# Kernel optimization log

Measured on AMD Instinct MI355X. Metric: run time of the kernel, lower is better.

Reference implementation:

```python
import jax, jax.numpy as jnp
import numpy as np

EPS = 1e-6  # VN-ReLU direction-norm epsilon
K_NN = 16


def vec_linear(x, W):
    # x: (B, Cin, 3, ...), W: (Cout, Cin) -> (B, Cout, 3, ...)
    return jnp.einsum('oi,bi...->bo...', W, x)


def vec_lna(x, W, U):
    # VecLinear + VN-LeakyReLU(negative_slope=0) acting on vector dim (axis 2)
    p = jnp.einsum('oi,bi...->bo...', W, x)   # feature map
    d = jnp.einsum('oi,bi...->bo...', U, x)   # direction map
    dot = jnp.sum(p * d, axis=2, keepdims=True)
    dsq = jnp.sum(d * d, axis=2, keepdims=True)
    return jnp.where(dot >= 0, p, p - (dot / (dsq + EPS)) * d)


def setup_inputs() -> dict:
    B, N = 2, 4096
    h, c, L = 128, 128, 4
    ks = jax.random.split(jax.random.key(0), 8)
    s = lambda k, shape, fan: (jax.random.normal(k, shape, jnp.float32) / np.sqrt(fan)).astype(jnp.float32)
    return {
        'x': jax.random.normal(ks[0], (B, 3, N), jnp.float32),
        'W_in': s(ks[1], (h, 3), 3),
        'U_in': s(ks[2], (h, 3), 3),
        'Wl': s(ks[3], (L, h, h), h),
        'Ul': s(ks[4], (L, h, h), h),
        'Wg': s(ks[5], (L, h, 2 * h), 2 * h),
        'Ug': s(ks[6], (L, h, 2 * h), 2 * h),
        'W_out': s(ks[7], (c, L * h), L * h),
    }


def reference(x, W_in, U_in, Wl, Ul, Wg, Ug, W_out):
    B, _, N = x.shape
    K = K_NN
    pts = jnp.transpose(x, (0, 2, 1))                      # (B, N, 3)
    # squared euclidean distance (same KNN ordering as torch.cdist p=2 + topk smallest)
    sq = jnp.sum(pts * pts, axis=-1)                       # (B, N)
    d2 = sq[:, :, None] + sq[:, None, :] - 2.0 * jnp.einsum('bnd,bmd->bnm', pts, pts)
    _, idx = jax.lax.top_k(-d2, K)                         # (B, N, K) nearest, sorted
    neighbors = jax.vmap(lambda p, i: p[i])(pts, idx)      # (B, N, K, 3) gather
    neighbors = jnp.transpose(neighbors, (0, 3, 1, 2))[:, None]  # (B, 1, 3, N, K)

    x4 = x[:, None]                                        # (B, 1, 3, N)
    x_pad = jnp.broadcast_to(x4[..., None], neighbors.shape)
    # F.normalize(x, dim=2) with eps=1e-12 clamp
    x_dir = x4 / jnp.maximum(jnp.linalg.norm(x4, axis=2, keepdims=True), 1e-12)
    cross = jnp.cross(jnp.broadcast_to(x_dir[..., None], neighbors.shape), neighbors, axis=2)
    y = jnp.concatenate([cross, neighbors - x_pad, x_pad], axis=1)  # (B, 3, 3, N, K)

    h_feat = vec_lna(y, W_in, U_in)                        # (B, h, 3, N, K)
    h_feat = jnp.mean(h_feat, axis=-1)                     # meanpool over K -> (B, h, 3, N)

    y = h_feat
    feats = []
    for i in range(Wl.shape[0]):
        y = vec_lna(y, Wl[i], Ul[i])                       # (B, h, 3, N)
        yg = jnp.mean(y, axis=-1, keepdims=True)
        y = jnp.concatenate([y, jnp.broadcast_to(yg, y.shape)], axis=1)  # (B, 2h, 3, N)
        y = vec_lna(y, Wg[i], Ug[i])                       # (B, h, 3, N)
        feats.append(y)

    out = vec_linear(jnp.concatenate(feats, axis=1), W_out)  # (B, c, 3, N)
    return (jnp.mean(out, axis=-1), out)
```

## Files before the change

### kernel.cpp

```cpp
#include <hip/hip_runtime.h>
#include <hip/hip_bf16.h>
#include <cfloat>


typedef __attribute__((ext_vector_type(8))) short short8;
typedef __attribute__((ext_vector_type(4))) float f32x4;

__device__ __forceinline__ unsigned short f2bf(float f) {
    union { float f; unsigned u; } v; v.f = f;
    unsigned r = v.u + 0x7fffu + ((v.u >> 16) & 1u);
    return (unsigned short)(r >> 16);
}
__device__ __forceinline__ float bf2f(unsigned short h) {
    union { unsigned u; float f; } v; v.u = ((unsigned)h) << 16;
    return v.f;
}

__global__ __launch_bounds__(256) void setup_kernel(const float* __restrict__ x,
                                                    float4* __restrict__ pts4,
                                                    const float* __restrict__ Wl,
                                                    const float* __restrict__ Ul,
                                                    const float* __restrict__ Wg,
                                                    const float* __restrict__ Ug,
                                                    const float* __restrict__ Wout,
                                                    unsigned short* __restrict__ Ah,
                                                    unsigned short* __restrict__ Al,
                                                    int N, int B) {
    int t = blockIdx.x * 256 + threadIdx.x;
    if (t < B * N) {
        int b = t / N, n = t - b * N;
        const float* xb = x + (long)b * 3 * N;
        float px = xb[n], py = xb[N + n], pz = xb[2 * N + n];
        pts4[t] = make_float4(px, py, pz, px * px + py * py + pz * pz);
    }
    int g, r, M; long base;
    if (t < 262144) { g = t >> 15; r = t & 32767; M = 256; base = (long)g << 15; }
    else { int t2 = t - 262144; g = 8 + (t2 >> 14); r = t2 & 16383; M = 128;
           base = 262144 + (long)(g - 8) * 16384; }
    int MF = M >> 4;
    int ks = r / (MF * 512);
    int mf = (r >> 9) % MF;
    int lane = (r >> 3) & 63;
    int j = r & 7;
    int m = mf * 16 + (lane & 15);
    int k = ks * 32 + ((lane >> 4) << 3) + j;
    const float* src; int ldw; int row;
    if (g < 4) {
        ldw = 128; row = m & 127;
        src = (m < 128) ? (Wl + (long)g * 128 * 128) : (Ul + (long)g * 128 * 128);
    } else if (g < 8) {
        ldw = 256; row = m & 127;
        int l = g - 4;
        src = (m < 128) ? (Wg + (long)l * 128 * 256) : (Ug + (long)l * 128 * 256);
    } else {
        ldw = 512; row = m;
        src = Wout + (g - 8) * 128;
    }
    float v = src[(long)row * ldw + k];
    unsigned short h = f2bf(v);
    Ah[base + r] = h;
    Al[base + r] = f2bf(v - bf2f(h));
}

__global__ __launch_bounds__(1024) void knn_kernel(const float4* __restrict__ pts4,
                                                   int* __restrict__ idxOut, int N) {
    __shared__ float4 cbuf[4096];
    int t = threadIdx.x;
    int tilesPerB = N / 16;
    int b = blockIdx.x / tilesPerB;
    int q = (blockIdx.x % tilesPerB) * 16 + (t >> 6);
    int lane = t & 63;

    for (int i = t; i < N; i += 1024) cbuf[i] = pts4[b * N + i];
    __syncthreads();

    float4 Q = cbuf[q];
    unsigned ku; int ki;

    {
        float4 C = cbuf[lane];
        float dot = Q.x * C.x + Q.y * C.y + Q.z * C.z;
        float d2 = Q.w + C.w - 2.0f * dot;
        unsigned u = __float_as_uint(d2);
        u ^= (unsigned)((int)u >> 31) | 0x80000000u;
        double key = (double)u * 4096.0 + (double)lane;
#pragma unroll
        for (int k = 2; k <= 64; k <<= 1) {
#pragma unroll
            for (int j = k >> 1; j > 0; j >>= 1) {
                double other = __shfl_xor(key, j);
                bool takeMin = (((lane & j) == 0) == ((lane & k) == 0));
                double mn = fmin(key, other), mx = fmax(key, other);
                key = takeMin ? mn : mx;
            }
        }
        long long kl = (long long)key;
        ki = (int)(kl & 4095);
        ku = (unsigned)(kl >> 12);
    }
    unsigned Tu = (unsigned)__builtin_amdgcn_readlane((int)ku, 15);

    for (int c0 = 64; c0 < N; c0 += 64) {
        float4 C = cbuf[c0 + lane];
        float dot = Q.x * C.x + Q.y * C.y + Q.z * C.z;
        float d2 = Q.w + C.w - 2.0f * dot;
        unsigned u = __float_as_uint(d2);
        u ^= (unsigned)((int)u >> 31) | 0x80000000u;
        int ci = c0 + lane;
        unsigned long long mask = __ballot(u <= Tu);
        while (mask) {
            int src = __ffsll(mask) - 1;
            mask &= mask - 1;
            unsigned vu = (unsigned)__builtin_amdgcn_readlane((int)u, src);
            int      vi = __builtin_amdgcn_readlane(ci, src);
            unsigned kum1 = (unsigned)__builtin_amdgcn_update_dpp(
                                (int)ku, (int)ku, 0x111, 0xF, 0xF, false);
            int      kim1 = __builtin_amdgcn_update_dpp(
                                ki, ki, 0x111, 0xF, 0xF, false);
            if (lane == 0) { kum1 = 0u; kim1 = (-2147483647 - 1); }
            bool lem1 = (vu < kum1) || (vu == kum1 && vi < kim1);
            bool ltj  = (vu < ku)   || (vu == ku   && vi < ki);
            unsigned knu = lem1 ? kum1 : (ltj ? vu : ku);
            int      kni = lem1 ? kim1 : (ltj ? vi : ki);
            if (lane < 16) { ku = knu; ki = kni; }
        }
        Tu = (unsigned)__builtin_amdgcn_readlane((int)ku, 15);
    }
    if (lane < 16) idxOut[(b * N + q) * 16 + lane] = ki;
}

__global__ __launch_bounds__(512, 1) void edgegemm0_kernel(
    const float4* __restrict__ pts4, const int* __restrict__ idx,
    const float* __restrict__ Win, const float* __restrict__ Uin,
    const unsigned short* __restrict__ Aph, const unsigned short* __restrict__ Apl,
    unsigned short* __restrict__ Oh, unsigned short* __restrict__ Ol,
    float* __restrict__ part, int N)
{
    __shared__ float4 nbuf[32][16];
    __shared__ float4 cpt[32];
    __shared__ unsigned short flds[2][3][2][2048];
    int t = threadIdx.x;
    int lane = t & 63, w = t >> 6;
    int mg = w >> 1, ng = w & 1;
    int b = blockIdx.x >> 7;
    int tile = blockIdx.x & 127;
    int n0 = tile * 32;

    {
        int pl = t >> 4, k = t & 15;
        int nb = idx[(b * N + n0 + pl) * 16 + k];
        nbuf[pl][k] = pts4[b * N + nb];
        if (t < 32) cpt[t] = pts4[b * N + n0 + t];
    }
    __syncthreads();
    {
        int o = t & 127, grp = t >> 7;
        float w0 = Win[o * 3], w1 = Win[o * 3 + 1], w2 = Win[o * 3 + 2];
        float u0 = Uin[o * 3], u1 = Uin[o * 3 + 1], u2 = Uin[o * 3 + 2];
        for (int pl = grp * 8; pl < grp * 8 + 8; ++pl) {
            float4 c4 = cpt[pl];
            float inv = 1.0f / fmaxf(sqrtf(c4.w), 1e-12f);
            float ax = c4.x * inv, ay = c4.y * inv, az = c4.z * inv;
            float a0 = 0.f, a1 = 0.f, a2 = 0.f;
            for (int k = 0; k < 16; ++k) {
                float4 nb = nbuf[pl][k];
                float cr0 = ay * nb.z - az * nb.y;
                float cr1 = az * nb.x - ax * nb.z;
                float cr2 = ax * nb.y - ay * nb.x;
                float df0 = nb.x - c4.x, df1 = nb.y - c4.y, df2 = nb.z - c4.z;
                float P0 = w0 * cr0 + w1 * df0 + w2 * c4.x;
                float P1 = w0 * cr1 + w1 * df1 + w2 * c4.y;
                float P2 = w0 * cr2 + w1 * df2 + w2 * c4.z;
                float D0 = u0 * cr0 + u1 * df0 + u2 * c4.x;
                float D1 = u0 * cr1 + u1 * df1 + u2 * c4.y;
                float D2 = u0 * cr2 + u1 * df2 + u2 * c4.z;
                float dot = P0 * D0 + P1 * D1 + P2 * D2;
                float dsq = D0 * D0 + D1 * D1 + D2 * D2;
                if (dot < 0.0f) {
                    float s = dot / (dsq + 1e-6f);
                    P0 -= s * D0; P1 -= s * D1; P2 -= s * D2;
                }
                a0 += P0; a1 += P1; a2 += P2;
            }
            float vals[3] = { a0 * (1.0f / 16.0f), a1 * (1.0f / 16.0f), a2 * (1.0f / 16.0f) };
            int ngg = pl >> 4, col = pl & 15;
            int li = ((o >> 3) << 7) + (col << 3) + (o & 7);
#pragma unroll
            for (int c = 0; c < 3; ++c) {
                unsigned short hh = f2bf(vals[c]);
                flds[ngg][c][0][li] = hh;
                flds[ngg][c][1][li] = f2bf(vals[c] - bf2f(hh));
            }
        }
    }
    __syncthreads();

    int ncol = tile * 32 + ng * 16 + (lane & 15);
    f32x4 accP[2][3] = {};
    f32x4 accD[2][3] = {};
#pragma unroll
    for (int ks = 0; ks < 4; ++ks) {
        short8 bh[3], bl[3];
        int li = (((ks << 2) + (lane >> 4)) << 7) + ((lane & 15) << 3);
#pragma unroll
        for (int c = 0; c < 3; ++c) {
            bh[c] = *(const short8*)&flds[ng][c][0][li];
            bl[c] = *(const short8*)&flds[ng][c][1][li];
        }
#pragma unroll
        for (int pi = 0; pi < 2; ++pi) {
            int mf = 2 * mg + pi;
            long aoffP = (((long)ks * 16 + mf) * 64 + lane) * 8;
            short8 ahP = *(const short8*)(Aph + aoffP);
            short8 alP = *(const short8*)(Apl + aoffP);
#pragma unroll
            for (int c = 0; c < 3; ++c) {
                accP[pi][c] = __builtin_amdgcn_mfma_f32_16x16x32_bf16(ahP, bh[c], accP[pi][c], 0, 0, 0);
                accP[pi][c] = __builtin_amdgcn_mfma_f32_16x16x32_bf16(ahP, bl[c], accP[pi][c], 0, 0, 0);
                accP[pi][c] = __builtin_amdgcn_mfma_f32_16x16x32_bf16(alP, bh[c], accP[pi][c], 0, 0, 0);
            }
            long aoffD = (((long)ks * 16 + (8 + mf)) * 64 + lane) * 8;
            short8 ahD = *(const short8*)(Aph + aoffD);
            short8 alD = *(const short8*)(Apl + aoffD);
#pragma unroll
            for (int c = 0; c < 3; ++c) {
                accD[pi][c] = __builtin_amdgcn_mfma_f32_16x16x32_bf16(ahD, bh[c], accD[pi][c], 0, 0, 0);
                accD[pi][c] = __builtin_amdgcn_mfma_f32_16x16x32_bf16(ahD, bl[c], accD[pi][c], 0, 0, 0);
                accD[pi][c] = __builtin_amdgcn_mfma_f32_16x16x32_bf16(alD, bh[c], accD[pi][c], 0, 0, 0);
            }
        }
    }

#pragma unroll
    for (int pi = 0; pi < 2; ++pi) {
        int obase = 32 * mg + 16 * pi + ((lane >> 4) << 2);
        float Pv[3][4];
#pragma unroll
        for (int r = 0; r < 4; ++r) {
            float P[3], D[3];
#pragma unroll
            for (int c = 0; c < 3; ++c) { P[c] = accP[pi][c][r]; D[c] = accD[pi][c][r]; }
            float dot = P[0] * D[0] + P[1] * D[1] + P[2] * D[2];
            float dsq = D[0] * D[0] + D[1] * D[1] + D[2] * D[2];
            if (dot < 0.0f) {
                float s = dot / (dsq + 1e-6f);
                P[0] -= s * D[0]; P[1] -= s * D[1]; P[2] -= s * D[2];
            }
            Pv[0][r] = P[0]; Pv[1][r] = P[1]; Pv[2][r] = P[2];
        }
#pragma unroll
        for (int c = 0; c < 3; ++c) {
            unsigned short hs[4], ls[4];
#pragma unroll
            for (int r = 0; r < 4; ++r) {
                hs[r] = f2bf(Pv[c][r]);
                ls[r] = f2bf(Pv[c][r] - bf2f(hs[r]));
            }
            long ooff = ((long)(b * 3 + c) * N + ncol) * 128 + obase;
            *(ushort4*)(Oh + ooff) = make_ushort4(hs[0], hs[1], hs[2], hs[3]);
            *(ushort4*)(Ol + ooff) = make_ushort4(ls[0], ls[1], ls[2], ls[3]);
        }
#pragma unroll
        for (int c = 0; c < 3; ++c) {
#pragma unroll
            for (int r = 0; r < 4; ++r) {
                float v = Pv[c][r];
                v += __shfl_xor(v, 1);
                v += __shfl_xor(v, 2);
                v += __shfl_xor(v, 4);
                v += __shfl_xor(v, 8);
                if ((lane & 15) == 0)
                    part[((long)(b * 3 + c) * 256 + tile * 2 + ng) * 128 + (obase + r)] = v;
            }
        }
    }
}

template<bool HASNEXT>
__global__ __launch_bounds__(512, 1) void fused_kernel(
    const unsigned short* __restrict__ Aph, const unsigned short* __restrict__ Apl,
    long aOffG, long aOffOut, long aOffNext,
    unsigned short* __restrict__ y1h, unsigned short* __restrict__ y1l,
    const float* __restrict__ biasP, const float* __restrict__ biasD,
    float* __restrict__ Ofp, float* __restrict__ part, int accum)
{
    const int N = 4096;
    __shared__ unsigned short ylds[2][3][2][2048];
    int t = threadIdx.x;
    int lane = t & 63, w = t >> 6;
    int mg = w >> 1, ng = w & 1;
    int b = blockIdx.x >> 7;
    int tile = blockIdx.x & 127;
    int ncol = tile * 32 + ng * 16 + (lane & 15);
    int kq = (lane >> 4) << 3;

    {
        f32x4 accP[2][3] = {};
        f32x4 accD[2][3] = {};
        const unsigned short* AhB = Aph + aOffG;
        const unsigned short* AlB = Apl + aOffG;
#pragma unroll
        for (int ks = 0; ks < 4; ++ks) {
            short8 bh[3], bl[3];
#pragma unroll
            for (int c = 0; c < 3; ++c) {
                long boff = ((long)(b * 3 + c) * N + ncol) * 128 + ks * 32 + kq;
                bh[c] = *(const short8*)(y1h + boff);
                bl[c] = *(const short8*)(y1l + boff);
            }
#pragma unroll
            for (int pi = 0; pi < 2; ++pi) {
                int mf = 2 * mg + pi;
                long aoffP = (((long)ks * 16 + mf) * 64 + lane) * 8;
                short8 ahP = *(const short8*)(AhB + aoffP);
                short8 alP = *(const short8*)(AlB + aoffP);
#pragma unroll
                for (int c = 0; c < 3; ++c) {
                    accP[pi][c] = __builtin_amdgcn_mfma_f32_16x16x32_bf16(ahP, bh[c], accP[pi][c], 0, 0, 0);
                    accP[pi][c] = __builtin_amdgcn_mfma_f32_16x16x32_bf16(ahP, bl[c], accP[pi][c], 0, 0, 0);
                    accP[pi][c] = __builtin_amdgcn_mfma_f32_16x16x32_bf16(alP, bh[c], accP[pi][c], 0, 0, 0);
                }
                long aoffD = (((long)ks * 16 + (8 + mf)) * 64 + lane) * 8;
                short8 ahD = *(const short8*)(AhB + aoffD);
                short8 alD = *(const short8*)(AlB + aoffD);
#pragma unroll
                for (int c = 0; c < 3; ++c) {
                    accD[pi][c] = __builtin_amdgcn_mfma_f32_16x16x32_bf16(ahD, bh[c], accD[pi][c], 0, 0, 0);
                    accD[pi][c] = __builtin_amdgcn_mfma_f32_16x16x32_bf16(ahD, bl[c], accD[pi][c], 0, 0, 0);
                    accD[pi][c] = __builtin_amdgcn_mfma_f32_16x16x32_bf16(alD, bh[c], accD[pi][c], 0, 0, 0);
                }
            }
        }
#pragma unroll
        for (int pi = 0; pi < 2; ++pi) {
            int obase = 32 * mg + 16 * pi + ((lane >> 4) << 2);
            float Pv[3][4];
#pragma unroll
            for (int r = 0; r < 4; ++r) {
                int o = obase + r;
                float P[3], D[3];
#pragma unroll
                for (int c = 0; c < 3; ++c) {
                    long bb = ((long)(b * 128 + o)) * 3 + c;
                    P[c] = accP[pi][c][r] + biasP[bb];
                    D[c] = accD[pi][c][r] + biasD[bb];
                }
                float dot = P[0] * D[0] + P[1] * D[1] + P[2] * D[2];
                float dsq = D[0] * D[0] + D[1] * D[1] + D[2] * D[2];
                if (dot < 0.0f) {
                    float s = dot / (dsq + 1e-6f);
                    P[0] -= s * D[0]; P[1] -= s * D[1]; P[2] -= s * D[2];
                }
                Pv[0][r] = P[0]; Pv[1][r] = P[1]; Pv[2][r] = P[2];
            }
#pragma unroll
            for (int c = 0; c < 3; ++c) {
                unsigned short hs[4], ls[4];
#pragma unroll
                for (int r = 0; r < 4; ++r) {
                    hs[r] = f2bf(Pv[c][r]);
                    ls[r] = f2bf(Pv[c][r] - bf2f(hs[r]));
                }
                int li = ((obase >> 3) << 7) + ((lane & 15) << 3) + (obase & 7);
                *(ushort4*)&ylds[ng][c][0][li] = make_ushort4(hs[0], hs[1], hs[2], hs[3]);
                *(ushort4*)&ylds[ng][c][1][li] = make_ushort4(ls[0], ls[1], ls[2], ls[3]);
            }
        }
    }
    __syncthreads();

    {
        f32x4 accO[2][3] = {};
        const unsigned short* AoH = Aph + aOffOut;
        const unsigned short* AoL = Apl + aOffOut;
#pragma unroll
        for (int ks = 0; ks < 4; ++ks) {
            short8 yh[3], yl[3];
            int li = (((ks << 2) + (lane >> 4)) << 7) + ((lane & 15) << 3);
#pragma unroll
            for (int c = 0; c < 3; ++c) {
                yh[c] = *(const short8*)&ylds[ng][c][0][li];
                yl[c] = *(const short8*)&ylds[ng][c][1][li];
            }
#pragma unroll
            for (int pi = 0; pi < 2; ++pi) {
                int mf = 2 * mg + pi;
                long aoff = (((long)ks * 8 + mf) * 64 + lane) * 8;
                short8 ah = *(const short8*)(AoH + aoff);
                short8 al = *(const short8*)(AoL + aoff);
#pragma unroll
                for (int c = 0; c < 3; ++c) {
                    accO[pi][c] = __builtin_amdgcn_mfma_f32_16x16x32_bf16(ah, yh[c], accO[pi][c], 0, 0, 0);
                    accO[pi][c] = __builtin_amdgcn_mfma_f32_16x16x32_bf16(ah, yl[c], accO[pi][c], 0, 0, 0);
                    accO[pi][c] = __builtin_amdgcn_mfma_f32_16x16x32_bf16(al, yh[c], accO[pi][c], 0, 0, 0);
                }
            }
        }
#pragma unroll
        for (int pi = 0; pi < 2; ++pi) {
            int obase = 32 * mg + 16 * pi + ((lane >> 4) << 2);
            float Ov[3][4];
#pragma unroll
            for (int r = 0; r < 4; ++r) {
                int o = obase + r;
#pragma unroll
                for (int c = 0; c < 3; ++c) {
                    long off = ((long)(b * 128 + o) * 3 + c) * N + ncol;
                    float v = accO[pi][c][r];
                    if (accum) v += Ofp[off];
                    Ofp[off] = v;
                    Ov[c][r] = v;
                }
            }
            if (!HASNEXT) {
#pragma unroll
                for (int c = 0; c < 3; ++c) {
#pragma unroll
                    for (int r = 0; r < 4; ++r) {
                        float v = Ov[c][r];
                        v += __shfl_xor(v, 1);
                        v += __shfl_xor(v, 2);
                        v += __shfl_xor(v, 4);
                        v += __shfl_xor(v, 8);
                        if ((lane & 15) == 0)
                            part[((long)(b * 3 + c) * 256 + tile * 2 + ng) * 128 + (obase + r)] = v;
                    }
                }
            }
        }
    }

    if (HASNEXT) {
        f32x4 accP[2][3] = {};
        f32x4 accD[2][3] = {};
        const unsigned short* AnH = Aph + aOffNext;
        const unsigned short* AnL = Apl + aOffNext;
#pragma unroll
        for (int ks = 0; ks < 4; ++ks) {
            short8 bh[3], bl[3];
            int li = (((ks << 2) + (lane >> 4)) << 7) + ((lane & 15) << 3);
#pragma unroll
            for (int c = 0; c < 3; ++c) {
                bh[c] = *(const short8*)&ylds[ng][c][0][li];
                bl[c] = *(const short8*)&ylds[ng][c][1][li];
            }
#pragma unroll
            for (int pi = 0; pi < 2; ++pi) {
                int mf = 2 * mg + pi;
                long aoffP = (((long)ks * 16 + mf) * 64 + lane) * 8;
                short8 ahP = *(const short8*)(AnH + aoffP);
                short8 alP = *(const short8*)(AnL + aoffP);
#pragma unroll
                for (int c = 0; c < 3; ++c) {
                    accP[pi][c] = __builtin_amdgcn_mfma_f32_16x16x32_bf16(ahP, bh[c], accP[pi][c], 0, 0, 0);
                    accP[pi][c] = __builtin_amdgcn_mfma_f32_16x16x32_bf16(ahP, bl[c], accP[pi][c], 0, 0, 0);
                    accP[pi][c] = __builtin_amdgcn_mfma_f32_16x16x32_bf16(alP, bh[c], accP[pi][c], 0, 0, 0);
                }
                long aoffD = (((long)ks * 16 + (8 + mf)) * 64 + lane) * 8;
                short8 ahD = *(const short8*)(AnH + aoffD);
                short8 alD = *(const short8*)(AnL + aoffD);
#pragma unroll
                for (int c = 0; c < 3; ++c) {
                    accD[pi][c] = __builtin_amdgcn_mfma_f32_16x16x32_bf16(ahD, bh[c], accD[pi][c], 0, 0, 0);
                    accD[pi][c] = __builtin_amdgcn_mfma_f32_16x16x32_bf16(ahD, bl[c], accD[pi][c], 0, 0, 0);
                    accD[pi][c] = __builtin_amdgcn_mfma_f32_16x16x32_bf16(alD, bh[c], accD[pi][c], 0, 0, 0);
                }
            }
        }
#pragma unroll
        for (int pi = 0; pi < 2; ++pi) {
            int obase = 32 * mg + 16 * pi + ((lane >> 4) << 2);
            float Pv[3][4];
#pragma unroll
            for (int r = 0; r < 4; ++r) {
                float P[3], D[3];
#pragma unroll
                for (int c = 0; c < 3; ++c) { P[c] = accP[pi][c][r]; D[c] = accD[pi][c][r]; }
                float dot = P[0] * D[0] + P[1] * D[1] + P[2] * D[2];
                float dsq = D[0] * D[0] + D[1] * D[1] + D[2] * D[2];
                if (dot < 0.0f) {
                    float s = dot / (dsq + 1e-6f);
                    P[0] -= s * D[0]; P[1] -= s * D[1]; P[2] -= s * D[2];
                }
                Pv[0][r] = P[0]; Pv[1][r] = P[1]; Pv[2][r] = P[2];
            }
#pragma unroll
            for (int c = 0; c < 3; ++c) {
                unsigned short hs[4], ls[4];
#pragma unroll
                for (int r = 0; r < 4; ++r) {
                    hs[r] = f2bf(Pv[c][r]);
                    ls[r] = f2bf(Pv[c][r] - bf2f(hs[r]));
                }
                long ooff = ((long)(b * 3 + c) * N + ncol) * 128 + obase;
                *(ushort4*)(y1h + ooff) = make_ushort4(hs[0], hs[1], hs[2], hs[3]);
                *(ushort4*)(y1l + ooff) = make_ushort4(ls[0], ls[1], ls[2], ls[3]);
            }
#pragma unroll
            for (int c = 0; c < 3; ++c) {
#pragma unroll
                for (int r = 0; r < 4; ++r) {
                    float v = Pv[c][r];
                    v += __shfl_xor(v, 1);
                    v += __shfl_xor(v, 2);
                    v += __shfl_xor(v, 4);
                    v += __shfl_xor(v, 8);
                    if ((lane & 15) == 0)
                        part[((long)(b * 3 + c) * 256 + tile * 2 + ng) * 128 + (obase + r)] = v;
                }
            }
        }
    }
}

__global__ __launch_bounds__(1024) void ygredbias_kernel(const float* __restrict__ part,
                                                         const float* __restrict__ Wg,
                                                         const float* __restrict__ Ug,
                                                         float* __restrict__ biasP,
                                                         float* __restrict__ biasD) {
    __shared__ float red[8][128];
    __shared__ float ygs[128];
    int bc = blockIdx.x;
    int t = threadIdx.x;
    int o = t & 127, g = t >> 7;
    float s = 0.f;
    for (int seg = g * 32; seg < g * 32 + 32; ++seg)
        s += part[((long)bc * 256 + seg) * 128 + o];
    red[g][o] = s;
    __syncthreads();
    if (t < 128) {
        float r = 0.f;
#pragma unroll
        for (int k = 0; k < 8; ++k) r += red[k][t];
        ygs[t] = r * (1.0f / 4096.0f);
    }
    __syncthreads();
    if (t < 256) {
        int oo = t & 127; bool isD = t >= 128;
        const float* row = (isD ? Ug : Wg) + oo * 256 + 128;
        float s2 = 0.f;
        for (int i = 0; i < 128; ++i) s2 = fmaf(row[i], ygs[i], s2);
        int b = bc / 3, c = bc % 3;
        (isD ? biasD : biasP)[((long)(b * 128 + oo)) * 3 + c] = s2;
    }
}

__global__ __launch_bounds__(1024) void out0red_kernel(const float* __restrict__ part,
                                                       float* __restrict__ out0) {
    __shared__ float red[8][128];
    int bc = blockIdx.x;
    int t = threadIdx.x;
    int o = t & 127, g = t >> 7;
    float s = 0.f;
    for (int seg = g * 32; seg < g * 32 + 32; ++seg)
        s += part[((long)bc * 256 + seg) * 128 + o];
    red[g][o] = s;
    __syncthreads();
    if (t < 128) {
        float r = 0.f;
#pragma unroll
        for (int k = 0; k < 8; ++k) r += red[k][t];
        int b = bc / 3, c = bc % 3;
        out0[((long)(b * 128) + t) * 3 + c] = r * (1.0f / 4096.0f);
    }
}

extern "C" void kernel_launch(void* const* d_in, const int* in_sizes, int n_in,
                              void* d_out, int out_size, void* d_ws, size_t ws_size,
                              hipStream_t stream) {
    const float* x    = (const float*)d_in[0];
    const float* Win  = (const float*)d_in[1];
    const float* Uin  = (const float*)d_in[2];
    const float* Wl   = (const float*)d_in[3];
    const float* Ul   = (const float*)d_in[4];
    const float* Wg   = (const float*)d_in[5];
    const float* Ug   = (const float*)d_in[6];
    const float* Wout = (const float*)d_in[7];

    const int B = 2, N = 4096, H = 128;
    float* out0 = (float*)d_out;
    float* out1 = out0 + (long)B * H * 3;

    float* ws = (float*)d_ws;
    long off = 0;
    float4* pts4 = (float4*)ws;                  off += (long)B * N * 4;
    int* idx = (int*)(ws + off);                 off += (long)B * N * 16;
    const long ACT = (long)B * 3 * N * H;
    unsigned short* y1h = (unsigned short*)(ws + off);  off += ACT / 2;
    unsigned short* y1l = (unsigned short*)(ws + off);  off += ACT / 2;
    unsigned short* Aph = (unsigned short*)(ws + off);  off += 327680 / 2;
    unsigned short* Apl = (unsigned short*)(ws + off);  off += 327680 / 2;
    float* part  = ws + off;                     off += 6L * 256 * 128;
    float* biasP = ws + off;                     off += B * H * 3;
    float* biasD = ws + off;                     off += B * H * 3;

    setup_kernel<<<1280, 256, 0, stream>>>(x, pts4, Wl, Ul, Wg, Ug, Wout, Aph, Apl, N, B);
    knn_kernel<<<B * (N / 16), 1024, 0, stream>>>(pts4, idx, N);

    edgegemm0_kernel<<<256, 512, 0, stream>>>(pts4, idx, Win, Uin,
                                              Aph, Apl, y1h, y1l, part, N);

    for (int l = 0; l < 4; ++l) {
        ygredbias_kernel<<<6, 1024, 0, stream>>>(part,
            Wg + (long)l * H * 256, Ug + (long)l * H * 256, biasP, biasD);
        long aG = (long)(4 + l) * 32768;
        long aO = 262144 + (long)l * 16384;
        if (l < 3) {
            fused_kernel<true><<<256, 512, 0, stream>>>(
                Aph, Apl, aG, aO, (long)(l + 1) * 32768,
                y1h, y1l, biasP, biasD, out1, part, l > 0 ? 1 : 0);
        } else {
            fused_kernel<false><<<256, 512, 0, stream>>>(
                Aph, Apl, aG, aO, 0L,
                y1h, y1l, biasP, biasD, out1, part, 1);
        }
    }
    out0red_kernel<<<6, 1024, 0, stream>>>(part, out0);
}
```

Baseline: 250.6 us.

## Double threads per block in edge and fused GEMM kernels, one M-fragment per wave

Raises block size from 512 to 1024 threads in the edge GEMM and fused layer kernels. Each wave now owns a single 16-row output fragment instead of two, which halves per-wave accumulator registers and doubles the number of waves per block. With only 256 blocks on the device, this is meant to raise latency hiding and MFMA issue parallelism per CU. In exchange, each wave reloads the shared B fragments for less work, and the larger block may face register pressure limits at 1024 threads.

```diff
diff --git a/kernel.cpp b/kernel.cpp
--- a/kernel.cpp
+++ b/kernel.cpp
@@ -129,7 +129,7 @@
     if (lane < 16) idxOut[(b * N + q) * 16 + lane] = ki;
 }
 
-__global__ __launch_bounds__(512, 1) void edgegemm0_kernel(
+__global__ __launch_bounds__(1024) void edgegemm0_kernel(
     const float4* __restrict__ pts4, const int* __restrict__ idx,
     const float* __restrict__ Win, const float* __restrict__ Uin,
     const unsigned short* __restrict__ Aph, const unsigned short* __restrict__ Apl,
@@ -141,23 +141,24 @@
     __shared__ unsigned short flds[2][3][2][2048];
     int t = threadIdx.x;
     int lane = t & 63, w = t >> 6;
-    int mg = w >> 1, ng = w & 1;
+    int ng = w >> 3, wv = w & 7;
     int b = blockIdx.x >> 7;
     int tile = blockIdx.x & 127;
     int n0 = tile * 32;
 
-    {
+    if (t < 512) {
         int pl = t >> 4, k = t & 15;
         int nb = idx[(b * N + n0 + pl) * 16 + k];
         nbuf[pl][k] = pts4[b * N + nb];
-        if (t < 32) cpt[t] = pts4[b * N + n0 + t];
+    } else if (t < 544) {
+        cpt[t - 512] = pts4[b * N + n0 + (t - 512)];
     }
     __syncthreads();
     {
         int o = t & 127, grp = t >> 7;
         float w0 = Win[o * 3], w1 = Win[o * 3 + 1], w2 = Win[o * 3 + 2];
         float u0 = Uin[o * 3], u1 = Uin[o * 3 + 1], u2 = Uin[o * 3 + 2];
-        for (int pl = grp * 8; pl < grp * 8 + 8; ++pl) {
+        for (int pl = grp * 4; pl < grp * 4 + 4; ++pl) {
             float4 c4 = cpt[pl];
             float inv = 1.0f / fmaxf(sqrtf(c4.w), 1e-12f);
             float ax = c4.x * inv, ay = c4.y * inv, az = c4.z * inv;
@@ -196,8 +197,8 @@
     __syncthreads();
 
     int ncol = tile * 32 + ng * 16 + (lane & 15);
-    f32x4 accP[2][3] = {};
-    f32x4 accD[2][3] = {};
+    f32x4 accP[3] = {};
+    f32x4 accD[3] = {};
 #pragma unroll
     for (int ks = 0; ks < 4; ++ks) {
         short8 bh[3], bl[3];
@@ -207,77 +208,67 @@
             bh[c] = *(const short8*)&flds[ng][c][0][li];
             bl[c] = *(const short8*)&flds[ng][c][1][li];
         }
-#pragma unroll
-        for (int pi = 0; pi < 2; ++pi) {
-            int mf = 2 * mg + pi;
-            long aoffP = (((long)ks * 16 + mf) * 64 + lane) * 8;
-            short8 ahP = *(const short8*)(Aph + aoffP);
-            short8 alP = *(const short8*)(Apl + aoffP);
-#pragma unroll
-            for (int c = 0; c < 3; ++c) {
-                accP[pi][c] = __builtin_amdgcn_mfma_f32_16x16x32_bf16(ahP, bh[c], accP[pi][c], 0, 0, 0);
-                accP[pi][c] = __builtin_amdgcn_mfma_f32_16x16x32_bf16(ahP, bl[c], accP[pi][c], 0, 0, 0);
-                accP[pi][c] = __builtin_amdgcn_mfma_f32_16x16x32_bf16(alP, bh[c], accP[pi][c], 0, 0, 0);
-            }
-            long aoffD = (((long)ks * 16 + (8 + mf)) * 64 + lane) * 8;
-            short8 ahD = *(const short8*)(Aph + aoffD);
-            short8 alD = *(const short8*)(Apl + aoffD);
-#pragma unroll
-            for (int c = 0; c < 3; ++c) {
-                accD[pi][c] = __builtin_amdgcn_mfma_f32_16x16x32_bf16(ahD, bh[c], accD[pi][c], 0, 0, 0);
-                accD[pi][c] = __builtin_amdgcn_mfma_f32_16x16x32_bf16(ahD, bl[c], accD[pi][c], 0, 0, 0);
-                accD[pi][c] = __builtin_amdgcn_mfma_f32_16x16x32_bf16(alD, bh[c], accD[pi][c], 0, 0, 0);
-            }
-        }
-    }
-
-#pragma unroll
-    for (int pi = 0; pi < 2; ++pi) {
-        int obase = 32 * mg + 16 * pi + ((lane >> 4) << 2);
-        float Pv[3][4];
+        long aoffP = (((long)ks * 16 + wv) * 64 + lane) * 8;
+        short8 ahP = *(const short8*)(Aph + aoffP);
+        short8 alP = *(const short8*)(Apl + aoffP);
+#pragma unroll
+        for (int c = 0; c < 3; ++c) {
+            accP[c] = __builtin_amdgcn_mfma_f32_16x16x32_bf16(ahP, bh[c], accP[c], 0, 0, 0);
+            accP[c] = __builtin_amdgcn_mfma_f32_16x16x32_bf16(ahP, bl[c], accP[c], 0, 0, 0);
+            accP[c] = __builtin_amdgcn_mfma_f32_16x16x32_bf16(alP, bh[c], accP[c], 0, 0, 0);
+        }
+        long aoffD = (((long)ks * 16 + 8 + wv) * 64 + lane) * 8;
+        short8 ahD = *(const short8*)(Aph + aoffD);
+        short8 alD = *(const short8*)(Apl + aoffD);
+#pragma unroll
+        for (int c = 0; c < 3; ++c) {
+            accD[c] = __builtin_amdgcn_mfma_f32_16x16x32_bf16(ahD, bh[c], accD[c], 0, 0, 0);
+            accD[c] = __builtin_amdgcn_mfma_f32_16x16x32_bf16(ahD, bl[c], accD[c], 0, 0, 0);
+            accD[c] = __builtin_amdgcn_mfma_f32_16x16x32_bf16(alD, bh[c], accD[c], 0, 0, 0);
+        }
+    }
+
+    int obase = 16 * wv + ((lane >> 4) << 2);
+    float Pv[3][4];
+#pragma unroll
+    for (int r = 0; r < 4; ++r) {
+        float P[3], D[3];
+#pragma unroll
+        for (int c = 0; c < 3; ++c) { P[c] = accP[c][r]; D[c] = accD[c][r]; }
+        float dot = P[0] * D[0] + P[1] * D[1] + P[2] * D[2];
+        float dsq = D[0] * D[0] + D[1] * D[1] + D[2] * D[2];
+        if (dot < 0.0f) {
+            float s = dot / (dsq + 1e-6f);
+            P[0] -= s * D[0]; P[1] -= s * D[1]; P[2] -= s * D[2];
+        }
+        Pv[0][r] = P[0]; Pv[1][r] = P[1]; Pv[2][r] = P[2];
+    }
+#pragma unroll
+    for (int c = 0; c < 3; ++c) {
+        unsigned short hs[4], ls[4];
 #pragma unroll
         for (int r = 0; r < 4; ++r) {
-            float P[3], D[3];
-#pragma unroll
-            for (int c = 0; c < 3; ++c) { P[c] = accP[pi][c][r]; D[c] = accD[pi][c][r]; }
-            float dot = P[0] * D[0] + P[1] * D[1] + P[2] * D[2];
-            float dsq = D[0] * D[0] + D[1] * D[1] + D[2] * D[2];
-            if (dot < 0.0f) {
-                float s = dot / (dsq + 1e-6f);
-                P[0] -= s * D[0]; P[1] -= s * D[1]; P[2] -= s * D[2];
-            }
-            Pv[0][r] = P[0]; Pv[1][r] = P[1]; Pv[2][r] = P[2];
-        }
-#pragma unroll
-        for (int c = 0; c < 3; ++c) {
-            unsigned short hs[4], ls[4];
-#pragma unroll
-            for (int r = 0; r < 4; ++r) {
-                hs[r] = f2bf(Pv[c][r]);
-                ls[r] = f2bf(Pv[c][r] - bf2f(hs[r]));
-            }
-            long ooff = ((long)(b * 3 + c) * N + ncol) * 128 + obase;
-            *(ushort4*)(Oh + ooff) = make_ushort4(hs[0], hs[1], hs[2], hs[3]);
-            *(ushort4*)(Ol + ooff) = make_ushort4(ls[0], ls[1], ls[2], ls[3]);
-        }
-#pragma unroll
-        for (int c = 0; c < 3; ++c) {
-#pragma unroll
-            for (int r = 0; r < 4; ++r) {
-                float v = Pv[c][r];
-                v += __shfl_xor(v, 1);
-                v += __shfl_xor(v, 2);
-                v += __shfl_xor(v, 4);
-                v += __shfl_xor(v, 8);
-                if ((lane & 15) == 0)
-                    part[((long)(b * 3 + c) * 256 + tile * 2 + ng) * 128 + (obase + r)] = v;
-            }
+            hs[r] = f2bf(Pv[c][r]);
+            ls[r] = f2bf(Pv[c][r] - bf2f(hs[r]));
+        }
+        long ooff = ((long)(b * 3 + c) * N + ncol) * 128 + obase;
+        *(ushort4*)(Oh + ooff) = make_ushort4(hs[0], hs[1], hs[2], hs[3]);
+        *(ushort4*)(Ol + ooff) = make_ushort4(ls[0], ls[1], ls[2], ls[3]);
+#pragma unroll
+        for (int r = 0; r < 4; ++r) {
+            float v = Pv[c][r];
+            v += __shfl_xor(v, 1);
+            v += __shfl_xor(v, 2);
+            v += __shfl_xor(v, 4);
+            v += __shfl_xor(v, 8);
+            if ((lane & 15) == 0)
+                part[((long)(b * 3 + c) * 256 + tile * 2 + ng) * 128 + (obase + r)] = v;
         }
     }
 }
 
 template<bool HASNEXT>
-__global__ __launch_bounds__(512, 1) void fused_kernel(
+__global__ __launch_bounds__(1024) void fused_kernel(
     const unsigned short* __restrict__ Aph, const unsigned short* __restrict__ Apl,
     long aOffG, long aOffOut, long aOffNext,
     unsigned short* __restrict__ y1h, unsigned short* __restrict__ y1l,
@@ -288,15 +279,15 @@
     __shared__ unsigned short ylds[2][3][2][2048];
     int t = threadIdx.x;
     int lane = t & 63, w = t >> 6;
-    int mg = w >> 1, ng = w & 1;
+    int ng = w >> 3, wv = w & 7;
     int b = blockIdx.x >> 7;
     int tile = blockIdx.x & 127;
     int ncol = tile * 32 + ng * 16 + (lane & 15);
     int kq = (lane >> 4) << 3;
 
     {
-        f32x4 accP[2][3] = {};
-        f32x4 accD[2][3] = {};
+        f32x4 accP[3] = {};
+        f32x4 accD[3] = {};
         const unsigned short* AhB = Aph + aOffG;
         const unsigned short* AlB = Apl + aOffG;
 #pragma unroll
@@ -308,69 +299,62 @@
                 bh[c] = *(const short8*)(y1h + boff);
                 bl[c] = *(const short8*)(y1l + boff);
             }
-#pragma unroll
-            for (int pi = 0; pi < 2; ++pi) {
-                int mf = 2 * mg + pi;
-                long aoffP = (((long)ks * 16 + mf) * 64 + lane) * 8;
-                short8 ahP = *(const short8*)(AhB + aoffP);
-                short8 alP = *(const short8*)(AlB + aoffP);
-#pragma unroll
-                for (int c = 0; c < 3; ++c) {
-                    accP[pi][c] = __builtin_amdgcn_mfma_f32_16x16x32_bf16(ahP, bh[c], accP[pi][c], 0, 0, 0);
-                    accP[pi][c] = __builtin_amdgcn_mfma_f32_16x16x32_bf16(ahP, bl[c], accP[pi][c], 0, 0, 0);
-                    accP[pi][c] = __builtin_amdgcn_mfma_f32_16x16x32_bf16(alP, bh[c], accP[pi][c], 0, 0, 0);
-                }
-                long aoffD = (((long)ks * 16 + (8 + mf)) * 64 + lane) * 8;
-                short8 ahD = *(const short8*)(AhB + aoffD);
-                short8 alD = *(const short8*)(AlB + aoffD);
-#pragma unroll
-                for (int c = 0; c < 3; ++c) {
-                    accD[pi][c] = __builtin_amdgcn_mfma_f32_16x16x32_bf16(ahD, bh[c], accD[pi][c], 0, 0, 0);
-                    accD[pi][c] = __builtin_amdgcn_mfma_f32_16x16x32_bf16(ahD, bl[c], accD[pi][c], 0, 0, 0);
-                    accD[pi][c] = __builtin_amdgcn_mfma_f32_16x16x32_bf16(alD, bh[c], accD[pi][c], 0, 0, 0);
-                }
-            }
-        }
-#pragma unroll
-        for (int pi = 0; pi < 2; ++pi) {
-            int obase = 32 * mg + 16 * pi + ((lane >> 4) << 2);
-            float Pv[3][4];
+            long aoffP = (((long)ks * 16 + wv) * 64 + lane) * 8;
+            short8 ahP = *(const short8*)(AhB + aoffP);
+            short8 alP = *(const short8*)(AlB + aoffP);
+#pragma unroll
+            for (int c = 0; c < 3; ++c) {
+                accP[c] = __builtin_amdgcn_mfma_f32_16x16x32_bf16(ahP, bh[c], accP[c], 0, 0, 0);
+                accP[c] = __builtin_amdgcn_mfma_f32_16x16x32_bf16(ahP, bl[c], accP[c], 0, 0, 0);
+                accP[c] = __builtin_amdgcn_mfma_f32_16x16x32_bf16(alP, bh[c], accP[c], 0, 0, 0);
+            }
+            long aoffD = (((long)ks * 16 + 8 + wv) * 64 + lane) * 8;
+            short8 ahD = *(const short8*)(AhB + aoffD);
+            short8 alD = *(const short8*)(AlB + aoffD);
+#pragma unroll
+            for (int c = 0; c < 3; ++c) {
+                accD[c] = __builtin_amdgcn_mfma_f32_16x16x32_bf16(ahD, bh[c], accD[c], 0, 0, 0);
+                accD[c] = __builtin_amdgcn_mfma_f32_16x16x32_bf16(ahD, bl[c], accD[c], 0, 0, 0);
+                accD[c] = __builtin_amdgcn_mfma_f32_16x16x32_bf16(alD, bh[c], accD[c], 0, 0, 0);
+            }
+        }
+        int obase = 16 * wv + ((lane >> 4) << 2);
+        float Pv[3][4];
+#pragma unroll
+        for (int r = 0; r < 4; ++r) {
+            int o = obase + r;
+            float P[3], D[3];
+#pragma unroll
+            for (int c = 0; c < 3; ++c) {
+                long bb = ((long)(b * 128 + o)) * 3 + c;
+                P[c] = accP[c][r] + biasP[bb];
+                D[c] = accD[c][r] + biasD[bb];
+            }
+            float dot = P[0] * D[0] + P[1] * D[1] + P[2] * D[2];
+            float dsq = D[0] * D[0] + D[1] * D[1] + D[2] * D[2];
+            if (dot < 0.0f) {
+                float s = dot / (dsq + 1e-6f);
+                P[0] -= s * D[0]; P[1] -= s * D[1]; P[2] -= s * D[2];
+            }
+            Pv[0][r] = P[0]; Pv[1][r] = P[1]; Pv[2][r] = P[2];
+        }
+#pragma unroll
+        for (int c = 0; c < 3; ++c) {
+            unsigned short hs[4], ls[4];
 #pragma unroll
             for (int r = 0; r < 4; ++r) {
-                int o = obase + r;
-                float P[3], D[3];
-#pragma unroll
-                for (int c = 0; c < 3; ++c) {
-                    long bb = ((long)(b * 128 + o)) * 3 + c;
-                    P[c] = accP[pi][c][r] + biasP[bb];
-                    D[c] = accD[pi][c][r] + biasD[bb];
-                }
-                float dot = P[0] * D[0] + P[1] * D[1] + P[2] * D[2];
-                float dsq = D[0] * D[0] + D[1] * D[1] + D[2] * D[2];
-                if (dot < 0.0f) {
-                    float s = dot / (dsq + 1e-6f);
-                    P[0] -= s * D[0]; P[1] -= s * D[1]; P[2] -= s * D[2];
-                }
-                Pv[0][r] = P[0]; Pv[1][r] = P[1]; Pv[2][r] = P[2];
-            }
-#pragma unroll
-            for (int c = 0; c < 3; ++c) {
-                unsigned short hs[4], ls[4];
-#pragma unroll
-                for (int r = 0; r < 4; ++r) {
-                    hs[r] = f2bf(Pv[c][r]);
-                    ls[r] = f2bf(Pv[c][r] - bf2f(hs[r]));
-                }
-                int li = ((obase >> 3) << 7) + ((lane & 15) << 3) + (obase & 7);
-                *(ushort4*)&ylds[ng][c][0][li] = make_ushort4(hs[0], hs[1], hs[2], hs[3]);
-                *(ushort4*)&ylds[ng][c][1][li] = make_ushort4(ls[0], ls[1], ls[2], ls[3]);
-            }
+                hs[r] = f2bf(Pv[c][r]);
+                ls[r] = f2bf(Pv[c][r] - bf2f(hs[r]));
+            }
+            int li = ((obase >> 3) << 7) + ((lane & 15) << 3) + (obase & 7);
+            *(ushort4*)&ylds[ng][c][0][li] = make_ushort4(hs[0], hs[1], hs[2], hs[3]);
+            *(ushort4*)&ylds[ng][c][1][li] = make_ushort4(ls[0], ls[1], ls[2], ls[3]);
         }
     }
     __syncthreads();
 
     {
-        f32x4 accO[2][3] = {};
+        f32x4 accO[3] = {};
         const unsigned short* AoH = Aph + aOffOut;
         const unsigned short* AoL = Apl + aOffOut;
 #pragma unroll
@@ -382,125 +366,36 @@
                 yh[c] = *(const short8*)&ylds[ng][c][0][li];
                 yl[c] = *(const short8*)&ylds[ng][c][1][li];
             }
-#pragma unroll
-            for (int pi = 0; pi < 2; ++pi) {
-                int mf = 2 * mg + pi;
-                long aoff = (((long)ks * 8 + mf) * 64 + lane) * 8;
-                short8 ah = *(const short8*)(AoH + aoff);
-                short8 al = *(const short8*)(AoL + aoff);
-#pragma unroll
-                for (int c = 0; c < 3; ++c) {
-                    accO[pi][c] = __builtin_amdgcn_mfma_f32_16x16x32_bf16(ah, yh[c], accO[pi][c], 0, 0, 0);
-                    accO[pi][c] = __builtin_amdgcn_mfma_f32_16x16x32_bf16(ah, yl[c], accO[pi][c], 0, 0, 0);
-                    accO[pi][c] = __builtin_amdgcn_mfma_f32_16x16x32_bf16(al, yh[c], accO[pi][c], 0, 0, 0);
-                }
-            }
-        }
-#pragma unroll
-        for (int pi = 0; pi < 2; ++pi) {
-            int obase = 32 * mg + 16 * pi + ((lane >> 4) << 2);
-            float Ov[3][4];
-#pragma unroll
-            for (int r = 0; r < 4; ++r) {
-                int o = obase + r;
-#pragma unroll
-                for (int c = 0; c < 3; ++c) {
-                    long off = ((long)(b * 128 + o) * 3 + c) * N + ncol;
-                    float v = accO[pi][c][r];
-                    if (accum) v += Ofp[off];
-                    Ofp[off] = v;
-                    Ov[c][r] = v;
-                }
-            }
-            if (!HASNEXT) {
-#pragma unroll
-                for (int c = 0; c < 3; ++c) {
-#pragma unroll
-                    for (int r = 0; r < 4; ++r) {
-                        float v = Ov[c][r];
-                        v += __shfl_xor(v, 1);
-                        v += __shfl_xor(v, 2);
-                        v += __shfl_xor(v, 4);
-                        v += __shfl_xor(v, 8);
-                        if ((lane & 15) == 0)
-                            part[((long)(b * 3 + c) * 256 + tile * 2 + ng) * 128 + (obase + r)] = v;
-                    }
-                }
-            }
-        }
-    }
-
-    if (HASNEXT) {
-        f32x4 accP[2][3] = {};
-        f32x4 accD[2][3] = {};
-        const unsigned short* AnH = Aph + aOffNext;
-        const unsigned short* AnL = Apl + aOffNext;
-#pragma unroll
-        for (int ks = 0; ks < 4; ++ks) {
-            short8 bh[3], bl[3];
-            int li = (((ks << 2) + (lane >> 4)) << 7) + ((lane & 15) << 3);
-#pragma unroll
-            for (int c = 0; c < 3; ++c) {
-                bh[c] = *(const short8*)&ylds[ng][c][0][li];
-                bl[c] = *(const short8*)&ylds[ng][c][1][li];
-            }
-#pragma unroll
-            for (int pi = 0; pi < 2; ++pi) {
-                int mf = 2 * mg + pi;
-                long aoffP = (((long)ks * 16 + mf) * 64 + lane) * 8;
-                short8 ahP = *(const short8*)(AnH + aoffP);
-                short8 alP = *(const short8*)(AnL + aoffP);
-#pragma unroll
-                for (int c = 0; c < 3; ++c) {
-                    accP[pi][c] = __builtin_amdgcn_mfma_f32_16x16x32_bf16(ahP, bh[c], accP[pi][c], 0, 0, 0);
-                    accP[pi][c] = __builtin_amdgcn_mfma_f32_16x16x32_bf16(ahP, bl[c], accP[pi][c], 0, 0, 0);
-                    accP[pi][c] = __builtin_amdgcn_mfma_f32_16x16x32_bf16(alP, bh[c], accP[pi][c], 0, 0, 0);
-                }
-                long aoffD = (((long)ks * 16 + (8 + mf)) * 64 + lane) * 8;
-                short8 ahD = *(const short8*)(AnH + aoffD);
-                short8 alD = *(const short8*)(AnL + aoffD);
-#pragma unroll
-                for (int c = 0; c < 3; ++c) {
-                    accD[pi][c] = __builtin_amdgcn_mfma_f32_16x16x32_bf16(ahD, bh[c], accD[pi][c], 0, 0, 0);
-                    accD[pi][c] = __builtin_amdgcn_mfma_f32_16x16x32_bf16(ahD, bl[c], accD[pi][c], 0, 0, 0);
-                    accD[pi][c] = __builtin_amdgcn_mfma_f32_16x16x32_bf16(alD, bh[c], accD[pi][c], 0, 0, 0);
-                }
-            }
-        }
-#pragma unroll
-        for (int pi = 0; pi < 2; ++pi) {
-            int obase = 32 * mg + 16 * pi + ((lane >> 4) << 2);
-            float Pv[3][4];
-#pragma unroll
-            for (int r = 0; r < 4; ++r) {
-                float P[3], D[3];
-#pragma unroll
-                for (int c = 0; c < 3; ++c) { P[c] = accP[pi][c][r]; D[c] = accD[pi][c][r]; }
-                float dot = P[0] * D[0] + P[1] * D[1] + P[2] * D[2];
-                float dsq = D[0] * D[0] + D[1] * D[1] + D[2] * D[2];
-                if (dot < 0.0f) {
-                    float s = dot / (dsq + 1e-6f);
-                    P[0] -= s * D[0]; P[1] -= s * D[1]; P[2] -= s * D[2];
-                }
-                Pv[0][r] = P[0]; Pv[1][r] = P[1]; Pv[2][r] = P[2];
-            }
-#pragma unroll
-            for (int c = 0; c < 3; ++c) {
-                unsigned short hs[4], ls[4];
+            long aoff = (((long)ks * 8 + wv) * 64 + lane) * 8;
+            short8 ah = *(const short8*)(AoH + aoff);
+            short8 al = *(const short8*)(AoL + aoff);
+#pragma unroll
+            for (int c = 0; c < 3; ++c) {
+                accO[c] = __builtin_amdgcn_mfma_f32_16x16x32_bf16(ah, yh[c], accO[c], 0, 0, 0);
+                accO[c] = __builtin_amdgcn_mfma_f32_16x16x32_bf16(ah, yl[c], accO[c], 0, 0, 0);
+                accO[c] = __builtin_amdgcn_mfma_f32_16x16x32_bf16(al, yh[c], accO[c], 0, 0, 0);
+            }
+        }
+        int obase = 16 * wv + ((lane >> 4) << 2);
+        float Ov[3][4];
+#pragma unroll
+        for (int r = 0; r < 4; ++r) {
+            int o = obase + r;
+#pragma unroll
+            for (int c = 0; c < 3; ++c) {
+                long off = ((long)(b * 128 + o) * 3 + c) * N + ncol;
+                float v = accO[c][r];
+                if (accum) v += Ofp[off];
+                Ofp[off] = v;
+                Ov[c][r] = v;
+            }
+        }
+        if (!HASNEXT) {
+#pragma unroll
+            for (int c = 0; c < 3; ++c) {
 #pragma unroll
                 for (int r = 0; r < 4; ++r) {
-                    hs[r] = f2bf(Pv[c][r]);
-                    ls[r] = f2bf(Pv[c][r] - bf2f(hs[r]));
-                }
-                long ooff = ((long)(b * 3 + c) * N + ncol) * 128 + obase;
-                *(ushort4*)(y1h + ooff) = make_ushort4(hs[0], hs[1], hs[2], hs[3]);
-                *(ushort4*)(y1l + ooff) = make_ushort4(ls[0], ls[1], ls[2], ls[3]);
-            }
-#pragma unroll
-            for (int c = 0; c < 3; ++c) {
-#pragma unroll
-                for (int r = 0; r < 4; ++r) {
-                    float v = Pv[c][r];
+                    float v = Ov[c][r];
                     v += __shfl_xor(v, 1);
                     v += __shfl_xor(v, 2);
                     v += __shfl_xor(v, 4);
@@ -508,6 +403,78 @@
                     if ((lane & 15) == 0)
                         part[((long)(b * 3 + c) * 256 + tile * 2 + ng) * 128 + (obase + r)] = v;
                 }
+            }
+        }
+    }
+
+    if (HASNEXT) {
+        f32x4 accP[3] = {};
+        f32x4 accD[3] = {};
+        const unsigned short* AnH = Aph + aOffNext;
+        const unsigned short* AnL = Apl + aOffNext;
+#pragma unroll
+        for (int ks = 0; ks < 4; ++ks) {
+            short8 bh[3], bl[3];
+            int li = (((ks << 2) + (lane >> 4)) << 7) + ((lane & 15) << 3);
+#pragma unroll
+            for (int c = 0; c < 3; ++c) {
+                bh[c] = *(const short8*)&ylds[ng][c][0][li];
+                bl[c] = *(const short8*)&ylds[ng][c][1][li];
+            }
+            long aoffP = (((long)ks * 16 + wv) * 64 + lane) * 8;
+            short8 ahP = *(const short8*)(AnH + aoffP);
+            short8 alP = *(const short8*)(AnL + aoffP);
+#pragma unroll
+            for (int c = 0; c < 3; ++c) {
+                accP[c] = __builtin_amdgcn_mfma_f32_16x16x32_bf16(ahP, bh[c], accP[c], 0, 0, 0);
+                accP[c] = __builtin_amdgcn_mfma_f32_16x16x32_bf16(ahP, bl[c], accP[c], 0, 0, 0);
+                accP[c] = __builtin_amdgcn_mfma_f32_16x16x32_bf16(alP, bh[c], accP[c], 0, 0, 0);
+            }
+            long aoffD = (((long)ks * 16 + 8 + wv) * 64 + lane) * 8;
+            short8 ahD = *(const short8*)(AnH + aoffD);
+            short8 alD = *(const short8*)(AnL + aoffD);
+#pragma unroll
+            for (int c = 0; c < 3; ++c) {
+                accD[c] = __builtin_amdgcn_mfma_f32_16x16x32_bf16(ahD, bh[c], accD[c], 0, 0, 0);
+                accD[c] = __builtin_amdgcn_mfma_f32_16x16x32_bf16(ahD, bl[c], accD[c], 0, 0, 0);
+                accD[c] = __builtin_amdgcn_mfma_f32_16x16x32_bf16(alD, bh[c], accD[c], 0, 0, 0);
+            }
+        }
+        int obase = 16 * wv + ((lane >> 4) << 2);
+        float Pv[3][4];
+#pragma unroll
+        for (int r = 0; r < 4; ++r) {
+            float P[3], D[3];
+#pragma unroll
+            for (int c = 0; c < 3; ++c) { P[c] = accP[c][r]; D[c] = accD[c][r]; }
+            float dot = P[0] * D[0] + P[1] * D[1] + P[2] * D[2];
+            float dsq = D[0] * D[0] + D[1] * D[1] + D[2] * D[2];
+            if (dot < 0.0f) {
+                float s = dot / (dsq + 1e-6f);
+                P[0] -= s * D[0]; P[1] -= s * D[1]; P[2] -= s * D[2];
+            }
+            Pv[0][r] = P[0]; Pv[1][r] = P[1]; Pv[2][r] = P[2];
+        }
+#pragma unroll
+        for (int c = 0; c < 3; ++c) {
+            unsigned short hs[4], ls[4];
+#pragma unroll
+            for (int r = 0; r < 4; ++r) {
+                hs[r] = f2bf(Pv[c][r]);
+                ls[r] = f2bf(Pv[c][r] - bf2f(hs[r]));
+            }
+            long ooff = ((long)(b * 3 + c) * N + ncol) * 128 + obase;
+            *(ushort4*)(y1h + ooff) = make_ushort4(hs[0], hs[1], hs[2], hs[3]);
+            *(ushort4*)(y1l + ooff) = make_ushort4(ls[0], ls[1], ls[2], ls[3]);
+#pragma unroll
+            for (int r = 0; r < 4; ++r) {
+                float v = Pv[c][r];
+                v += __shfl_xor(v, 1);
+                v += __shfl_xor(v, 2);
+                v += __shfl_xor(v, 4);
+                v += __shfl_xor(v, 8);
+                if ((lane & 15) == 0)
+                    part[((long)(b * 3 + c) * 256 + tile * 2 + ng) * 128 + (obase + r)] = v;
             }
         }
     }
@@ -597,8 +564,8 @@
     setup_kernel<<<1280, 256, 0, stream>>>(x, pts4, Wl, Ul, Wg, Ug, Wout, Aph, Apl, N, B);
     knn_kernel<<<B * (N / 16), 1024, 0, stream>>>(pts4, idx, N);
 
-    edgegemm0_kernel<<<256, 512, 0, stream>>>(pts4, idx, Win, Uin,
-                                              Aph, Apl, y1h, y1l, part, N);
+    edgegemm0_kernel<<<256, 1024, 0, stream>>>(pts4, idx, Win, Uin,
+                                               Aph, Apl, y1h, y1l, part, N);
 
     for (int l = 0; l < 4; ++l) {
         ygredbias_kernel<<<6, 1024, 0, stream>>>(part,
@@ -606,11 +573,11 @@
         long aG = (long)(4 + l) * 32768;
         long aO = 262144 + (long)l * 16384;
         if (l < 3) {
-            fused_kernel<true><<<256, 512, 0, stream>>>(
+            fused_kernel<true><<<256, 1024, 0, stream>>>(
                 Aph, Apl, aG, aO, (long)(l + 1) * 32768,
                 y1h, y1l, biasP, biasD, out1, part, l > 0 ? 1 : 0);
         } else {
-            fused_kernel<false><<<256, 512, 0, stream>>>(
+            fused_kernel<false><<<256, 1024, 0, stream>>>(
                 Aph, Apl, aG, aO, 0L,
                 y1h, y1l, biasP, biasD, out1, part, 1);
         }
```

New measurement: 231.3 us, median of 2. 1.08x faster.
